# Kernel tuning notes

Measured on AMD Instinct MI355X. Metric: run time of the kernel, lower is better.

Reference implementation:

```python
import jax, jax.numpy as jnp
import numpy as np

N_NODES = 100000
N_EDGES = 3200000
IN_CH = 24
HIDDEN = 64
N_CLASSES = 16


def _sage_conv(x, src, dst, W_l, b_l, W_r, num_nodes):
    # mean-aggregate neighbor features at destination nodes
    msg = x[src]                                             # [E, F] gather
    agg = jax.ops.segment_sum(msg, dst, num_segments=num_nodes)
    deg = jax.ops.segment_sum(jnp.ones((src.shape[0],), x.dtype), dst,
                              num_segments=num_nodes)
    mean = agg / jnp.maximum(deg, 1.0)[:, None]
    # PyG SAGEConv: lin_l(aggregated) + lin_r(self); bias lives in lin_l
    return mean @ W_l.T + b_l + x @ W_r.T


def setup_inputs() -> dict:
    key = jax.random.key(0)
    ks = jax.random.split(key, 8)
    x = jax.random.normal(ks[0], (N_NODES, IN_CH), dtype=jnp.float32)
    edge_index = jax.random.randint(ks[1], (2, N_EDGES), 0, N_NODES, dtype=jnp.int64)
    s1 = 1.0 / np.sqrt(IN_CH)
    s2 = 1.0 / np.sqrt(HIDDEN)
    return {
        "x": x,
        "edge_index": edge_index,
        "W1_l": jax.random.normal(ks[2], (HIDDEN, IN_CH), dtype=jnp.float32) * s1,
        "b1": jnp.zeros((HIDDEN,), jnp.float32),
        "W1_r": jax.random.normal(ks[3], (HIDDEN, IN_CH), dtype=jnp.float32) * s1,
        "W2_l": jax.random.normal(ks[4], (HIDDEN, HIDDEN), dtype=jnp.float32) * s2,
        "b2": jnp.zeros((HIDDEN,), jnp.float32),
        "W2_r": jax.random.normal(ks[5], (HIDDEN, HIDDEN), dtype=jnp.float32) * s2,
        "Wc": jax.random.normal(ks[6], (N_CLASSES, HIDDEN), dtype=jnp.float32) * s2,
        "bc": jnp.zeros((N_CLASSES,), jnp.float32),
    }


def reference(x, edge_index, W1_l, b1, W1_r, W2_l, b2, W2_r, Wc, bc):
    num_nodes = x.shape[0]
    src, dst = edge_index[0], edge_index[1]
    h = _sage_conv(x, src, dst, W1_l, b1, W1_r, num_nodes)
    h = jax.nn.relu(h)
    # dropout is identity in eval mode
    embeddings = _sage_conv(h, src, dst, W2_l, b2, W2_r, num_nodes)
    logits = embeddings @ Wc.T + bc
    return (logits, embeddings)
```

## Files before the change

### kernel.cpp

```cpp
#include <hip/hip_runtime.h>

#define N_NODES 100000
#define N_EDGES 3200000
#define IN_CH 24
#define HIDDEN 64
#define N_CLASSES 16

#define NBUCK 782
#define CAP 4608
#define PTBLOCKS 256
#define PTCHUNK 12500

typedef __attribute__((ext_vector_type(8))) short short8;
typedef __attribute__((ext_vector_type(4))) float float4_;
typedef __attribute__((ext_vector_type(2))) float float2v;
typedef __attribute__((ext_vector_type(4))) int int4v;
typedef __attribute__((ext_vector_type(2))) unsigned uint2v;

__device__ unsigned llvm_amdgcn_raw_buffer_load_u32(int4v, int, int, int) __asm("llvm.amdgcn.raw.buffer.load.i32");
__device__ uint2v llvm_amdgcn_raw_buffer_load_u32x2(int4v, int, int, int) __asm("llvm.amdgcn.raw.buffer.load.v2i32");

__device__ __forceinline__ int4v make_srd(const void* p, unsigned bytes) {
    unsigned long long a = (unsigned long long)p;
    int4v r;
    r.x = (int)(unsigned)a;
    r.y = (int)((unsigned)(a >> 32) & 0xFFFFu);
    r.z = (int)bytes;
    r.w = 0x00020000;
    return r;
}

__device__ __forceinline__ unsigned short f2bf(float f) {
    union { float f; unsigned int u; } v; v.f = f;
    unsigned int u = v.u;
    return (unsigned short)((u + 0x7FFFu + ((u >> 16) & 1u)) >> 16);
}
__device__ __forceinline__ unsigned cvt_pk_bf16(float a, float b) {
    unsigned r;
    asm("v_cvt_pk_bf16_f32 %0, %1, %2" : "=v"(r) : "v"(a), "v"(b));
    return r;
}
__device__ __forceinline__ unsigned short pk_fp8(float a, float b) {
    return (unsigned short)(__builtin_amdgcn_cvt_pk_fp8_f32(a, b, 0, false) & 0xFFFF);
}
__device__ __forceinline__ void accum_dw(float2v* A, unsigned w) {
    A[0] += __builtin_amdgcn_cvt_pk_f32_fp8(w, false);
    A[1] += __builtin_amdgcn_cvt_pk_f32_fp8(w, true);
}
__device__ __forceinline__ short8 mk8(unsigned d0, unsigned d1, unsigned d2, unsigned d3) {
    union { unsigned u[4]; short8 s; } v;
    v.u[0] = d0; v.u[1] = d1; v.u[2] = d2; v.u[3] = d3;
    return v.s;
}


__global__ __launch_bounds__(256) void k_prep(const float* __restrict__ W1l,
                                              const float* __restrict__ W1r,
                                              const float* __restrict__ W2l,
                                              const float* __restrict__ W2r,
                                              const float* __restrict__ Wc,
                                              const float* __restrict__ b2,
                                              const float* __restrict__ bc,
                                              unsigned short* __restrict__ Bt1,
                                              unsigned short* __restrict__ Bt2,
                                              float* __restrict__ bias2,
                                              int* __restrict__ bucketFill) {
    int t = threadIdx.x;
    for (int i = t; i < NBUCK; i += 256) bucketFill[i] = 0;
    for (int i = t; i < 64 * 64; i += 256) {
        int o = i >> 6, k = i & 63;
        float v = (k < 24) ? W1r[o * 24 + k] : ((k < 48) ? W1l[o * 24 + k - 24] : 0.f);
        Bt1[i] = f2bf(v);
    }
    for (int i = t; i < 64 * 128; i += 256) {
        int o = i >> 7, k = i & 127;
        float v = (k < 64) ? W2l[o * 64 + k] : W2r[o * 64 + k - 64];
        Bt2[i] = f2bf(v);
    }
    for (int i = t; i < 16 * 128; i += 256) {
        int c = i >> 7, k = i & 127;
        const float* M = (k < 64) ? W2l : W2r;
        int kk = k & 63;
        float s = 0.f;
        for (int j = 0; j < 64; j++) s += Wc[c * 64 + j] * M[j * 64 + kk];
        Bt2[(64 + c) * 128 + k] = f2bf(s);
    }
    for (int i = t; i < 80; i += 256) {
        if (i < 64) bias2[i] = b2[i];
        else {
            int c = i - 64;
            float s = bc[c];
            for (int j = 0; j < 64; j++) s += Wc[c * 64 + j] * b2[j];
            bias2[i] = s;
        }
    }
}


__global__ __launch_bounds__(1024) void k_part(const int* __restrict__ src,
                                               const int* __restrict__ dst,
                                               int* __restrict__ bucketFill,
                                               unsigned int* __restrict__ pedges) {
    __shared__ int cntL[NBUCK];
    __shared__ int baseL[NBUCK];
    int t = threadIdx.x;
    int cbeg = blockIdx.x * PTCHUNK;
    int d[13], s[13];
#pragma unroll
    for (int k = 0; k < 13; k++) {
        int o = k * 1024 + t;
        bool ok = o < PTCHUNK;
        d[k] = ok ? dst[cbeg + o] : -1;
        s[k] = ok ? src[cbeg + o] : 0;
    }
    for (int i = t; i < NBUCK; i += 1024) cntL[i] = 0;
    __syncthreads();
#pragma unroll
    for (int k = 0; k < 13; k++)
        if (d[k] >= 0) atomicAdd(&cntL[d[k] >> 7], 1);
    __syncthreads();
    for (int i = t; i < NBUCK; i += 1024) {
        int c = cntL[i];
        if (c) baseL[i] = i * CAP + atomicAdd(&bucketFill[i], c);
        cntL[i] = 0;
    }
    __syncthreads();
#pragma unroll
    for (int k = 0; k < 13; k++)
        if (d[k] >= 0) {
            int bk = d[k] >> 7;
            int r = atomicAdd(&cntL[bk], 1);
            pedges[baseL[bk] + r] = ((unsigned int)(d[k] & 127) << 17) | (unsigned int)s[k];
        }
}

__global__ __launch_bounds__(1024) void k_bucket(const unsigned int* __restrict__ pedges,
                                                 const int* __restrict__ bucketFill,
                                                 int2* __restrict__ begend,
                                                 int* __restrict__ srcs, int N) {
    __shared__ int ncnt[128];
    __shared__ int sps[128];
    int b = blockIdx.x;
    int t = threadIdx.x;
    int eb0 = b * CAP;
    int m = bucketFill[b];
    unsigned int v[5];
#pragma unroll
    for (int k = 0; k < 5; k++) {
        int o = k * 1024 + t;
        v[k] = (o < m) ? pedges[eb0 + o] : 0xFFFFFFFFu;
    }
    if (t < 128) ncnt[t] = 0;
    __syncthreads();
#pragma unroll
    for (int k = 0; k < 5; k++)
        if (v[k] != 0xFFFFFFFFu) atomicAdd(&ncnt[v[k] >> 17], 1);
    __syncthreads();
    int myc = (t < 128) ? ncnt[t] : 0;
    int val = myc;
    if (t < 128) sps[t] = val;
    __syncthreads();
    for (int off = 1; off < 128; off <<= 1) {
        int vv = (t >= off && t < 128) ? sps[t - off] : 0;
        __syncthreads();
        if (t < 128) { val += vv; sps[t] = val; }
        __syncthreads();
    }
    int mybase = val - myc;
    int node = b * 128 + t;
    if (t < 128 && node < N) {
        int2 be; be.x = eb0 + mybase; be.y = eb0 + mybase + myc;
        begend[node] = be;
    }
    if (t < 128) { sps[t] = mybase; ncnt[t] = 0; }
    if (t < 32) srcs[eb0 + m + t] = 0;
    __syncthreads();
#pragma unroll
    for (int k = 0; k < 5; k++)
        if (v[k] != 0xFFFFFFFFu) {
            unsigned int nl = v[k] >> 17;
            int r = atomicAdd(&ncnt[nl], 1);
            srcs[eb0 + sps[nl] + r] = (int)(v[k] & 0x1FFFF);
        }
}

__global__ __launch_bounds__(256) void k_castx(const float* __restrict__ x,
                                               unsigned short* __restrict__ X8s) {
    int gid = blockIdx.x * 256 + threadIdx.x;
    if (gid >= N_NODES * 16) return;
    int n = gid >> 4, kp = gid & 15;
    if (kp < 12) {
        const float2 v = *(const float2*)(x + n * 24 + kp * 2);
        X8s[n * 16 + kp] = pk_fp8(v.x, v.y);
    } else {
        X8s[n * 16 + kp] = 0;
    }
}


__global__ __launch_bounds__(256) void k_fuse1(const float* __restrict__ x,
                                               const unsigned int* __restrict__ X8u,
                                               const int2* __restrict__ begend,
                                               const int* __restrict__ srcs,
                                               const unsigned short* __restrict__ Bt1,
                                               const float* __restrict__ b1,
                                               unsigned short* __restrict__ A2s,
                                               unsigned char* __restrict__ H8b) {
    __shared__ unsigned int lds_mean[16][20];
    int w = threadIdx.x >> 6;
    int lane = threadIdx.x & 63;
    int base = blockIdx.x * 16;
    int grp = lane >> 3;
    int sub = lane & 7;
    const int4v srdX = make_srd(X8u, N_NODES * 32u);
    const int4v srdS = make_srd(srcs, (unsigned)NBUCK * CAP * 4u);
    int suboff = sub * 4;

    for (int i = 0; i < 4; i++) {
        int il = w * 4 + i;
        int2 be = begend[base + il];
        int b = be.x, e = be.y;
        float2v A[2] = {{0.f, 0.f}, {0.f, 0.f}};
        int nfull = (e - b) & ~31;
        int j = b;
        int vo = (b + grp) * 4;
        for (; j < b + nfull; j += 32, vo += 128) {
            int s0 = (int)llvm_amdgcn_raw_buffer_load_u32(srdS, vo, 0, 0);
            int s1 = (int)llvm_amdgcn_raw_buffer_load_u32(srdS, vo + 32, 0, 0);
            int s2 = (int)llvm_amdgcn_raw_buffer_load_u32(srdS, vo + 64, 0, 0);
            int s3 = (int)llvm_amdgcn_raw_buffer_load_u32(srdS, vo + 96, 0, 0);
            unsigned u0 = llvm_amdgcn_raw_buffer_load_u32(srdX, (s0 << 5) + suboff, 0, 0);
            unsigned u1 = llvm_amdgcn_raw_buffer_load_u32(srdX, (s1 << 5) + suboff, 0, 0);
            unsigned u2 = llvm_amdgcn_raw_buffer_load_u32(srdX, (s2 << 5) + suboff, 0, 0);
            unsigned u3 = llvm_amdgcn_raw_buffer_load_u32(srdX, (s3 << 5) + suboff, 0, 0);
            accum_dw(A, u0); accum_dw(A, u1); accum_dw(A, u2); accum_dw(A, u3);
        }
        if (j < e) {
            int j0 = j + grp;
            int s0 = (int)llvm_amdgcn_raw_buffer_load_u32(srdS, vo, 0, 0);
            int s1 = (int)llvm_amdgcn_raw_buffer_load_u32(srdS, vo + 32, 0, 0);
            int s2 = (int)llvm_amdgcn_raw_buffer_load_u32(srdS, vo + 64, 0, 0);
            int s3 = (int)llvm_amdgcn_raw_buffer_load_u32(srdS, vo + 96, 0, 0);
            int o0 = (j0 < e)      ? ((s0 << 5) + suboff) : 0x7FFF0000;
            int o1 = (j0 + 8 < e)  ? ((s1 << 5) + suboff) : 0x7FFF0000;
            int o2 = (j0 + 16 < e) ? ((s2 << 5) + suboff) : 0x7FFF0000;
            int o3 = (j0 + 24 < e) ? ((s3 << 5) + suboff) : 0x7FFF0000;
            unsigned u0 = llvm_amdgcn_raw_buffer_load_u32(srdX, o0, 0, 0);
            unsigned u1 = llvm_amdgcn_raw_buffer_load_u32(srdX, o1, 0, 0);
            unsigned u2 = llvm_amdgcn_raw_buffer_load_u32(srdX, o2, 0, 0);
            unsigned u3 = llvm_amdgcn_raw_buffer_load_u32(srdX, o3, 0, 0);
            accum_dw(A, u0); accum_dw(A, u1); accum_dw(A, u2); accum_dw(A, u3);
        }
#pragma unroll
        for (int mm = 8; mm <= 32; mm <<= 1) {
#pragma unroll
            for (int q = 0; q < 2; q++) {
                float2v t;
                t.x = __shfl_xor(A[q].x, mm, 64);
                t.y = __shfl_xor(A[q].y, mm, 64);
                A[q] += t;
            }
        }
        if (lane < 8) {
            float inv = __builtin_amdgcn_rcpf((float)max(e - b, 1));
            lds_mean[il][sub * 2]     = cvt_pk_bf16(A[0].x * inv, A[0].y * inv);
            lds_mean[il][sub * 2 + 1] = cvt_pk_bf16(A[1].x * inv, A[1].y * inv);
        }
    }
    __syncthreads();

    int m = lane & 15, quad = lane >> 4;
    int row = base + m;
    short8 bf0 = *(const short8*)(Bt1 + (w * 16 + m) * 64 + quad * 8);
    short8 bf1 = *(const short8*)(Bt1 + (w * 16 + m) * 64 + 32 + quad * 8);
    float bias = b1[w * 16 + m];
    short8 a0, a1;
    if (quad < 3) {
        const float4* xp = (const float4*)(x + row * 24 + quad * 8);
        float4 v0 = xp[0], v1 = xp[1];
        a0 = mk8(cvt_pk_bf16(v0.x, v0.y), cvt_pk_bf16(v0.z, v0.w),
                 cvt_pk_bf16(v1.x, v1.y), cvt_pk_bf16(v1.z, v1.w));
    } else {
        a0 = *(const short8*)&lds_mean[m][0];
    }
    if (quad == 0)      a1 = *(const short8*)&lds_mean[m][4];
    else if (quad == 1) a1 = *(const short8*)&lds_mean[m][8];
    else                a1 = mk8(0u, 0u, 0u, 0u);
    float4_ c = {0.f, 0.f, 0.f, 0.f};
    c = __builtin_amdgcn_mfma_f32_16x16x32_bf16(a0, bf0, c, 0, 0, 0);
    c = __builtin_amdgcn_mfma_f32_16x16x32_bf16(a1, bf1, c, 0, 0, 0);
    int col = w * 16 + m;
#pragma unroll
    for (int r = 0; r < 4; r++) {
        int row2 = base + quad * 4 + r;
        float v = fmaxf(c[r] + bias, 0.f);
        A2s[row2 * 128 + 64 + col] = f2bf(v);
        H8b[row2 * 64 + col] =
            (unsigned char)(__builtin_amdgcn_cvt_pk_fp8_f32(v, 0.f, 0, false) & 0xFF);
    }
}

__global__ __launch_bounds__(256) void k_fuse2(const unsigned int* __restrict__ H8u,
                                               const int2* __restrict__ begend,
                                               const int* __restrict__ srcs,
                                               const unsigned short* __restrict__ Bt2,
                                               const float* __restrict__ bias2,
                                               unsigned short* A2s,
                                               float* __restrict__ logits) {
    __shared__ unsigned int lds_h[16][36];
    int w = threadIdx.x >> 6;
    int lane = threadIdx.x & 63;
    int base = blockIdx.x * 16;
    int grp = lane >> 3;
    int sub = lane & 7;
    const int4v srdH = make_srd(H8u, N_NODES * 64u);
    const int4v srdS = make_srd(srcs, (unsigned)NBUCK * CAP * 4u);
    int suboff = sub * 8;

    for (int i = 0; i < 4; i++) {
        int il = w * 4 + i;
        int2 be = begend[base + il];
        int b = be.x, e = be.y;
        float2v A[4] = {{0.f, 0.f}, {0.f, 0.f}, {0.f, 0.f}, {0.f, 0.f}};
        int nfull = (e - b) & ~31;
        int j = b;
        int vo = (b + grp) * 4;
        for (; j < b + nfull; j += 32, vo += 128) {
            int s0 = (int)llvm_amdgcn_raw_buffer_load_u32(srdS, vo, 0, 0);
            int s1 = (int)llvm_amdgcn_raw_buffer_load_u32(srdS, vo + 32, 0, 0);
            int s2 = (int)llvm_amdgcn_raw_buffer_load_u32(srdS, vo + 64, 0, 0);
            int s3 = (int)llvm_amdgcn_raw_buffer_load_u32(srdS, vo + 96, 0, 0);
            uint2v u0 = llvm_amdgcn_raw_buffer_load_u32x2(srdH, (s0 << 6) + suboff, 0, 0);
            uint2v u1 = llvm_amdgcn_raw_buffer_load_u32x2(srdH, (s1 << 6) + suboff, 0, 0);
            uint2v u2 = llvm_amdgcn_raw_buffer_load_u32x2(srdH, (s2 << 6) + suboff, 0, 0);
            uint2v u3 = llvm_amdgcn_raw_buffer_load_u32x2(srdH, (s3 << 6) + suboff, 0, 0);
            accum_dw(A, u0.x); accum_dw(A + 2, u0.y);
            accum_dw(A, u1.x); accum_dw(A + 2, u1.y);
            accum_dw(A, u2.x); accum_dw(A + 2, u2.y);
            accum_dw(A, u3.x); accum_dw(A + 2, u3.y);
        }
        if (j < e) {
            int j0 = j + grp;
            int s0 = (int)llvm_amdgcn_raw_buffer_load_u32(srdS, vo, 0, 0);
            int s1 = (int)llvm_amdgcn_raw_buffer_load_u32(srdS, vo + 32, 0, 0);
            int s2 = (int)llvm_amdgcn_raw_buffer_load_u32(srdS, vo + 64, 0, 0);
            int s3 = (int)llvm_amdgcn_raw_buffer_load_u32(srdS, vo + 96, 0, 0);
            int o0 = (j0 < e)      ? ((s0 << 6) + suboff) : 0x7FFF0000;
            int o1 = (j0 + 8 < e)  ? ((s1 << 6) + suboff) : 0x7FFF0000;
            int o2 = (j0 + 16 < e) ? ((s2 << 6) + suboff) : 0x7FFF0000;
            int o3 = (j0 + 24 < e) ? ((s3 << 6) + suboff) : 0x7FFF0000;
            uint2v u0 = llvm_amdgcn_raw_buffer_load_u32x2(srdH, o0, 0, 0);
            uint2v u1 = llvm_amdgcn_raw_buffer_load_u32x2(srdH, o1, 0, 0);
            uint2v u2 = llvm_amdgcn_raw_buffer_load_u32x2(srdH, o2, 0, 0);
            uint2v u3 = llvm_amdgcn_raw_buffer_load_u32x2(srdH, o3, 0, 0);
            accum_dw(A, u0.x); accum_dw(A + 2, u0.y);
            accum_dw(A, u1.x); accum_dw(A + 2, u1.y);
            accum_dw(A, u2.x); accum_dw(A + 2, u2.y);
            accum_dw(A, u3.x); accum_dw(A + 2, u3.y);
        }
#pragma unroll
        for (int mm = 8; mm <= 32; mm <<= 1) {
#pragma unroll
            for (int q = 0; q < 4; q++) {
                float2v t;
                t.x = __shfl_xor(A[q].x, mm, 64);
                t.y = __shfl_xor(A[q].y, mm, 64);
                A[q] += t;
            }
        }
        if (lane < 8) {
            float inv = __builtin_amdgcn_rcpf((float)max(e - b, 1));
            uint4 o;
            o.x = cvt_pk_bf16(A[0].x * inv, A[0].y * inv);
            o.y = cvt_pk_bf16(A[1].x * inv, A[1].y * inv);
            o.z = cvt_pk_bf16(A[2].x * inv, A[2].y * inv);
            o.w = cvt_pk_bf16(A[3].x * inv, A[3].y * inv);
            *(uint4*)&lds_h[il][sub * 4] = o;
        }
    }
    __syncthreads();

    int m = lane & 15, quad = lane >> 4;
    int row = base + m;
    short8 a0 = *(const short8*)&lds_h[m][quad * 4];
    short8 a1 = *(const short8*)&lds_h[m][16 + quad * 4];
    short8 a2 = *(const short8*)(A2s + row * 128 + 64 + quad * 8);
    short8 a3 = *(const short8*)(A2s + row * 128 + 96 + quad * 8);
    short8 bf[4], bg[4];
#pragma unroll
    for (int s = 0; s < 4; s++)
        bf[s] = *(const short8*)(Bt2 + (w * 16 + m) * 128 + s * 32 + quad * 8);
    float bias = bias2[w * 16 + m];
    float bias4 = 0.f;
    if (w == 3) {
#pragma unroll
        for (int s = 0; s < 4; s++)
            bg[s] = *(const short8*)(Bt2 + (64 + m) * 128 + s * 32 + quad * 8);
        bias4 = bias2[64 + m];
    }
    __syncthreads();
    float4_ c = {0.f, 0.f, 0.f, 0.f};
    c = __builtin_amdgcn_mfma_f32_16x16x32_bf16(a0, bf[0], c, 0, 0, 0);
    c = __builtin_amdgcn_mfma_f32_16x16x32_bf16(a1, bf[1], c, 0, 0, 0);
    c = __builtin_amdgcn_mfma_f32_16x16x32_bf16(a2, bf[2], c, 0, 0, 0);
    c = __builtin_amdgcn_mfma_f32_16x16x32_bf16(a3, bf[3], c, 0, 0, 0);
    float* embp = (float*)A2s;
    int col = w * 16 + m;
#pragma unroll
    for (int r = 0; r < 4; r++) {
        int row2 = base + quad * 4 + r;
        embp[row2 * 64 + col] = c[r] + bias;
    }
    if (w == 3) {
        float4_ cl = {0.f, 0.f, 0.f, 0.f};
        cl = __builtin_amdgcn_mfma_f32_16x16x32_bf16(a0, bg[0], cl, 0, 0, 0);
        cl = __builtin_amdgcn_mfma_f32_16x16x32_bf16(a1, bg[1], cl, 0, 0, 0);
        cl = __builtin_amdgcn_mfma_f32_16x16x32_bf16(a2, bg[2], cl, 0, 0, 0);
        cl = __builtin_amdgcn_mfma_f32_16x16x32_bf16(a3, bg[3], cl, 0, 0, 0);
#pragma unroll
        for (int r = 0; r < 4; r++) {
            int row2 = base + quad * 4 + r;
            logits[row2 * 16 + m] = cl[r] + bias4;
        }
    }
}


extern "C" void kernel_launch(void* const* d_in, const int* in_sizes, int n_in,
                              void* d_out, int out_size, void* d_ws, size_t ws_size,
                              hipStream_t stream) {
    const float* x = (const float*)d_in[0];
    const int* edge = (const int*)d_in[1];
    const int* srcIdx = edge;
    const int* dstIdx = edge + N_EDGES;
    const float* W1l = (const float*)d_in[2];
    const float* b1  = (const float*)d_in[3];
    const float* W1r = (const float*)d_in[4];
    const float* W2l = (const float*)d_in[5];
    const float* b2  = (const float*)d_in[6];
    const float* W2r = (const float*)d_in[7];
    const float* Wc  = (const float*)d_in[8];
    const float* bc  = (const float*)d_in[9];

    float* logits = (float*)d_out;
    unsigned short* A2s = (unsigned short*)((float*)d_out + (size_t)N_NODES * N_CLASSES);

    char* w = (char*)d_ws;
    auto carve = [&](size_t bytes) {
        char* p = w;
        w += (bytes + 255) & ~(size_t)255;
        return p;
    };
    int2* begend         = (int2*)carve((size_t)N_NODES * sizeof(int2));
    int* srcs            = (int*)carve((size_t)NBUCK * CAP * sizeof(int));
    unsigned int* pedges = (unsigned int*)carve((size_t)NBUCK * CAP * sizeof(unsigned int));
    unsigned short* X8s  = (unsigned short*)carve((size_t)N_NODES * 32);
    unsigned char* H8b   = (unsigned char*)carve((size_t)N_NODES * 64);
    int* bucketFill      = (int*)carve(NBUCK * sizeof(int));
    unsigned short* Bt1  = (unsigned short*)carve(64 * 64 * sizeof(unsigned short));
    unsigned short* Bt2  = (unsigned short*)carve(80 * 128 * sizeof(unsigned short));
    float* bias2         = (float*)carve(80 * sizeof(float));

    unsigned int* X8u = (unsigned int*)X8s;
    unsigned int* H8u = (unsigned int*)H8b;

    k_prep<<<1, 256, 0, stream>>>(W1l, W1r, W2l, W2r, Wc, b2, bc, Bt1, Bt2, bias2,
                                  bucketFill);
    k_part<<<PTBLOCKS, 1024, 0, stream>>>(srcIdx, dstIdx, bucketFill, pedges);
    k_bucket<<<NBUCK, 1024, 0, stream>>>(pedges, bucketFill, begend, srcs, N_NODES);
    k_castx<<<(N_NODES * 16 + 255) / 256, 256, 0, stream>>>(x, X8s);

    int fgrid = N_NODES / 16;
    k_fuse1<<<fgrid, 256, 0, stream>>>(x, X8u, begend, srcs, Bt1, b1, A2s, H8b);
    k_fuse2<<<fgrid, 256, 0, stream>>>(H8u, begend, srcs, Bt2, bias2, A2s, logits);
}
```

Before: 264.4 us.

## Merge prep/cast into partition launch and use one wave per node in fused layers

Folds the weight-prep and x-to-fp8 cast kernels into extra blocks of the partition kernel and replaces the bucket-fill zeroing with a memset, cutting launch count and letting the cast overlap the partitioning. The fused aggregation kernels move from 4 waves each handling 4 nodes sequentially to 16 waves each handling one node. This raises memory-level parallelism in the gathers, but most waves sit idle during the MFMA phase. In layer 2 a fifth wave now computes the logits in parallel instead of wave 3 doing them serially.

Result: slower. 272.5 us (+3.1%).

```diff
diff --git a/kernel.cpp b/kernel.cpp
--- a/kernel.cpp
+++ b/kernel.cpp
@@ -10,6 +10,7 @@
 #define CAP 4608
 #define PTBLOCKS 256
 #define PTCHUNK 12500
+#define NCASTB 1563
 
 typedef __attribute__((ext_vector_type(8))) short short8;
 typedef __attribute__((ext_vector_type(4))) float float4_;
@@ -54,57 +55,70 @@
 }
 
 
-__global__ __launch_bounds__(256) void k_prep(const float* __restrict__ W1l,
-                                              const float* __restrict__ W1r,
-                                              const float* __restrict__ W2l,
-                                              const float* __restrict__ W2r,
-                                              const float* __restrict__ Wc,
-                                              const float* __restrict__ b2,
-                                              const float* __restrict__ bc,
-                                              unsigned short* __restrict__ Bt1,
-                                              unsigned short* __restrict__ Bt2,
-                                              float* __restrict__ bias2,
-                                              int* __restrict__ bucketFill) {
-    int t = threadIdx.x;
-    for (int i = t; i < NBUCK; i += 256) bucketFill[i] = 0;
-    for (int i = t; i < 64 * 64; i += 256) {
-        int o = i >> 6, k = i & 63;
-        float v = (k < 24) ? W1r[o * 24 + k] : ((k < 48) ? W1l[o * 24 + k - 24] : 0.f);
-        Bt1[i] = f2bf(v);
-    }
-    for (int i = t; i < 64 * 128; i += 256) {
-        int o = i >> 7, k = i & 127;
-        float v = (k < 64) ? W2l[o * 64 + k] : W2r[o * 64 + k - 64];
-        Bt2[i] = f2bf(v);
-    }
-    for (int i = t; i < 16 * 128; i += 256) {
-        int c = i >> 7, k = i & 127;
-        const float* M = (k < 64) ? W2l : W2r;
-        int kk = k & 63;
-        float s = 0.f;
-        for (int j = 0; j < 64; j++) s += Wc[c * 64 + j] * M[j * 64 + kk];
-        Bt2[(64 + c) * 128 + k] = f2bf(s);
-    }
-    for (int i = t; i < 80; i += 256) {
-        if (i < 64) bias2[i] = b2[i];
-        else {
-            int c = i - 64;
-            float s = bc[c];
-            for (int j = 0; j < 64; j++) s += Wc[c * 64 + j] * b2[j];
-            bias2[i] = s;
-        }
-    }
-}
-
-
-__global__ __launch_bounds__(1024) void k_part(const int* __restrict__ src,
-                                               const int* __restrict__ dst,
-                                               int* __restrict__ bucketFill,
-                                               unsigned int* __restrict__ pedges) {
+__global__ __launch_bounds__(1024) void k_partx(const int* __restrict__ src,
+                                                const int* __restrict__ dst,
+                                                int* __restrict__ bucketFill,
+                                                unsigned int* __restrict__ pedges,
+                                                const float* __restrict__ x,
+                                                unsigned short* __restrict__ X8s,
+                                                const float* __restrict__ W1l,
+                                                const float* __restrict__ W1r,
+                                                const float* __restrict__ W2l,
+                                                const float* __restrict__ W2r,
+                                                const float* __restrict__ Wc,
+                                                const float* __restrict__ b2,
+                                                const float* __restrict__ bc,
+                                                unsigned short* __restrict__ Bt1,
+                                                unsigned short* __restrict__ Bt2,
+                                                float* __restrict__ bias2) {
     __shared__ int cntL[NBUCK];
     __shared__ int baseL[NBUCK];
     int t = threadIdx.x;
-    int cbeg = blockIdx.x * PTCHUNK;
+    int bid = blockIdx.x;
+    if (bid >= PTBLOCKS) {
+        if (bid < PTBLOCKS + NCASTB) {
+            int gid = (bid - PTBLOCKS) * 1024 + t;
+            if (gid >= N_NODES * 16) return;
+            int n = gid >> 4, kp = gid & 15;
+            if (kp < 12) {
+                const float2 v = *(const float2*)(x + n * 24 + kp * 2);
+                X8s[n * 16 + kp] = pk_fp8(v.x, v.y);
+            } else {
+                X8s[n * 16 + kp] = 0;
+            }
+        } else {
+            for (int i = t; i < 64 * 64; i += 1024) {
+                int o = i >> 6, k = i & 63;
+                float v = (k < 24) ? W1r[o * 24 + k]
+                                   : ((k < 48) ? W1l[o * 24 + k - 24] : 0.f);
+                Bt1[i] = f2bf(v);
+            }
+            for (int i = t; i < 64 * 128; i += 1024) {
+                int o = i >> 7, k = i & 127;
+                float v = (k < 64) ? W2l[o * 64 + k] : W2r[o * 64 + k - 64];
+                Bt2[i] = f2bf(v);
+            }
+            for (int i = t; i < 16 * 128; i += 1024) {
+                int c = i >> 7, k = i & 127;
+                const float* M = (k < 64) ? W2l : W2r;
+                int kk = k & 63;
+                float s = 0.f;
+                for (int j = 0; j < 64; j++) s += Wc[c * 64 + j] * M[j * 64 + kk];
+                Bt2[(64 + c) * 128 + k] = f2bf(s);
+            }
+            for (int i = t; i < 80; i += 1024) {
+                if (i < 64) bias2[i] = b2[i];
+                else {
+                    int c = i - 64;
+                    float s = bc[c];
+                    for (int j = 0; j < 64; j++) s += Wc[c * 64 + j] * b2[j];
+                    bias2[i] = s;
+                }
+            }
+        }
+        return;
+    }
+    int cbeg = bid * PTCHUNK;
     int d[13], s[13];
 #pragma unroll
     for (int k = 0; k < 13; k++) {
@@ -184,28 +198,15 @@
         }
 }
 
-__global__ __launch_bounds__(256) void k_castx(const float* __restrict__ x,
-                                               unsigned short* __restrict__ X8s) {
-    int gid = blockIdx.x * 256 + threadIdx.x;
-    if (gid >= N_NODES * 16) return;
-    int n = gid >> 4, kp = gid & 15;
-    if (kp < 12) {
-        const float2 v = *(const float2*)(x + n * 24 + kp * 2);
-        X8s[n * 16 + kp] = pk_fp8(v.x, v.y);
-    } else {
-        X8s[n * 16 + kp] = 0;
-    }
-}
-
-
-__global__ __launch_bounds__(256) void k_fuse1(const float* __restrict__ x,
-                                               const unsigned int* __restrict__ X8u,
-                                               const int2* __restrict__ begend,
-                                               const int* __restrict__ srcs,
-                                               const unsigned short* __restrict__ Bt1,
-                                               const float* __restrict__ b1,
-                                               unsigned short* __restrict__ A2s,
-                                               unsigned char* __restrict__ H8b) {
+
+__global__ __launch_bounds__(1024) void k_fuse1(const float* __restrict__ x,
+                                                const unsigned int* __restrict__ X8u,
+                                                const int2* __restrict__ begend,
+                                                const int* __restrict__ srcs,
+                                                const unsigned short* __restrict__ Bt1,
+                                                const float* __restrict__ b1,
+                                                unsigned short* __restrict__ A2s,
+                                                unsigned char* __restrict__ H8b) {
     __shared__ unsigned int lds_mean[16][20];
     int w = threadIdx.x >> 6;
     int lane = threadIdx.x & 63;
@@ -216,9 +217,8 @@
     const int4v srdS = make_srd(srcs, (unsigned)NBUCK * CAP * 4u);
     int suboff = sub * 4;
 
-    for (int i = 0; i < 4; i++) {
-        int il = w * 4 + i;
-        int2 be = begend[base + il];
+    {
+        int2 be = begend[base + w];
         int b = be.x, e = be.y;
         float2v A[2] = {{0.f, 0.f}, {0.f, 0.f}};
         int nfull = (e - b) & ~31;
@@ -263,11 +263,12 @@
         }
         if (lane < 8) {
             float inv = __builtin_amdgcn_rcpf((float)max(e - b, 1));
-            lds_mean[il][sub * 2]     = cvt_pk_bf16(A[0].x * inv, A[0].y * inv);
-            lds_mean[il][sub * 2 + 1] = cvt_pk_bf16(A[1].x * inv, A[1].y * inv);
-        }
-    }
-    __syncthreads();
+            lds_mean[w][sub * 2]     = cvt_pk_bf16(A[0].x * inv, A[0].y * inv);
+            lds_mean[w][sub * 2 + 1] = cvt_pk_bf16(A[1].x * inv, A[1].y * inv);
+        }
+    }
+    __syncthreads();
+    if (w >= 4) return;
 
     int m = lane & 15, quad = lane >> 4;
     int row = base + m;
@@ -300,13 +301,13 @@
     }
 }
 
-__global__ __launch_bounds__(256) void k_fuse2(const unsigned int* __restrict__ H8u,
-                                               const int2* __restrict__ begend,
-                                               const int* __restrict__ srcs,
-                                               const unsigned short* __restrict__ Bt2,
-                                               const float* __restrict__ bias2,
-                                               unsigned short* A2s,
-                                               float* __restrict__ logits) {
+__global__ __launch_bounds__(1024) void k_fuse2(const unsigned int* __restrict__ H8u,
+                                                const int2* __restrict__ begend,
+                                                const int* __restrict__ srcs,
+                                                const unsigned short* __restrict__ Bt2,
+                                                const float* __restrict__ bias2,
+                                                unsigned short* A2s,
+                                                float* __restrict__ logits) {
     __shared__ unsigned int lds_h[16][36];
     int w = threadIdx.x >> 6;
     int lane = threadIdx.x & 63;
@@ -317,9 +318,8 @@
     const int4v srdS = make_srd(srcs, (unsigned)NBUCK * CAP * 4u);
     int suboff = sub * 8;
 
-    for (int i = 0; i < 4; i++) {
-        int il = w * 4 + i;
-        int2 be = begend[base + il];
+    {
+        int2 be = begend[base + w];
         int b = be.x, e = be.y;
         float2v A[4] = {{0.f, 0.f}, {0.f, 0.f}, {0.f, 0.f}, {0.f, 0.f}};
         int nfull = (e - b) & ~31;
@@ -375,52 +375,47 @@
             o.y = cvt_pk_bf16(A[1].x * inv, A[1].y * inv);
             o.z = cvt_pk_bf16(A[2].x * inv, A[2].y * inv);
             o.w = cvt_pk_bf16(A[3].x * inv, A[3].y * inv);
-            *(uint4*)&lds_h[il][sub * 4] = o;
+            *(uint4*)&lds_h[w][sub * 4] = o;
         }
     }
     __syncthreads();
 
     int m = lane & 15, quad = lane >> 4;
     int row = base + m;
+    short8 a2, a3, bf[4];
+    float bias = 0.f;
+    bool doP2 = (w < 5);
+    if (doP2) {
+        int trow = ((w < 4) ? w * 16 : 64) + m;
+#pragma unroll
+        for (int s = 0; s < 4; s++)
+            bf[s] = *(const short8*)(Bt2 + trow * 128 + s * 32 + quad * 8);
+        bias = bias2[trow];
+        a2 = *(const short8*)(A2s + row * 128 + 64 + quad * 8);
+        a3 = *(const short8*)(A2s + row * 128 + 96 + quad * 8);
+    }
+    __syncthreads();
+    if (!doP2) return;
     short8 a0 = *(const short8*)&lds_h[m][quad * 4];
     short8 a1 = *(const short8*)&lds_h[m][16 + quad * 4];
-    short8 a2 = *(const short8*)(A2s + row * 128 + 64 + quad * 8);
-    short8 a3 = *(const short8*)(A2s + row * 128 + 96 + quad * 8);
-    short8 bf[4], bg[4];
-#pragma unroll
-    for (int s = 0; s < 4; s++)
-        bf[s] = *(const short8*)(Bt2 + (w * 16 + m) * 128 + s * 32 + quad * 8);
-    float bias = bias2[w * 16 + m];
-    float bias4 = 0.f;
-    if (w == 3) {
-#pragma unroll
-        for (int s = 0; s < 4; s++)
-            bg[s] = *(const short8*)(Bt2 + (64 + m) * 128 + s * 32 + quad * 8);
-        bias4 = bias2[64 + m];
-    }
-    __syncthreads();
     float4_ c = {0.f, 0.f, 0.f, 0.f};
     c = __builtin_amdgcn_mfma_f32_16x16x32_bf16(a0, bf[0], c, 0, 0, 0);
     c = __builtin_amdgcn_mfma_f32_16x16x32_bf16(a1, bf[1], c, 0, 0, 0);
     c = __builtin_amdgcn_mfma_f32_16x16x32_bf16(a2, bf[2], c, 0, 0, 0);
     c = __builtin_amdgcn_mfma_f32_16x16x32_bf16(a3, bf[3], c, 0, 0, 0);
-    float* embp = (float*)A2s;
-    int col = w * 16 + m;
-#pragma unroll
-    for (int r = 0; r < 4; r++) {
-        int row2 = base + quad * 4 + r;
-        embp[row2 * 64 + col] = c[r] + bias;
-    }
-    if (w == 3) {
-        float4_ cl = {0.f, 0.f, 0.f, 0.f};
-        cl = __builtin_amdgcn_mfma_f32_16x16x32_bf16(a0, bg[0], cl, 0, 0, 0);
-        cl = __builtin_amdgcn_mfma_f32_16x16x32_bf16(a1, bg[1], cl, 0, 0, 0);
-        cl = __builtin_amdgcn_mfma_f32_16x16x32_bf16(a2, bg[2], cl, 0, 0, 0);
-        cl = __builtin_amdgcn_mfma_f32_16x16x32_bf16(a3, bg[3], cl, 0, 0, 0);
+    if (w < 4) {
+        float* embp = (float*)A2s;
+        int col = w * 16 + m;
 #pragma unroll
         for (int r = 0; r < 4; r++) {
             int row2 = base + quad * 4 + r;
-            logits[row2 * 16 + m] = cl[r] + bias4;
+            embp[row2 * 64 + col] = c[r] + bias;
+        }
+    } else {
+#pragma unroll
+        for (int r = 0; r < 4; r++) {
+            int row2 = base + quad * 4 + r;
+            logits[row2 * 16 + m] = c[r] + bias;
         }
     }
 }
@@ -464,13 +459,13 @@
     unsigned int* X8u = (unsigned int*)X8s;
     unsigned int* H8u = (unsigned int*)H8b;
 
-    k_prep<<<1, 256, 0, stream>>>(W1l, W1r, W2l, W2r, Wc, b2, bc, Bt1, Bt2, bias2,
-                                  bucketFill);
-    k_part<<<PTBLOCKS, 1024, 0, stream>>>(srcIdx, dstIdx, bucketFill, pedges);
+    hipMemsetAsync(bucketFill, 0, NBUCK * sizeof(int), stream);
+    k_partx<<<PTBLOCKS + NCASTB + 1, 1024, 0, stream>>>(
+        srcIdx, dstIdx, bucketFill, pedges, x, X8s,
+        W1l, W1r, W2l, W2r, Wc, b2, bc, Bt1, Bt2, bias2);
     k_bucket<<<NBUCK, 1024, 0, stream>>>(pedges, bucketFill, begend, srcs, N_NODES);
-    k_castx<<<(N_NODES * 16 + 255) / 256, 256, 0, stream>>>(x, X8s);
 
     int fgrid = N_NODES / 16;
-    k_fuse1<<<fgrid, 256, 0, stream>>>(x, X8u, begend, srcs, Bt1, b1, A2s, H8b);
-    k_fuse2<<<fgrid, 256, 0, stream>>>(H8u, begend, srcs, Bt2, bias2, A2s, logits);
-}
+    k_fuse1<<<fgrid, 1024, 0, stream>>>(x, X8u, begend, srcs, Bt1, b1, A2s, H8b);
+    k_fuse2<<<fgrid, 1024, 0, stream>>>(H8u, begend, srcs, Bt2, bias2, A2s, logits);
+}
```
